# Kernel optimization log

Measured on AMD Instinct MI355X. Metric: run time of the kernel, lower is better.

Reference implementation:

```python
import jax, jax.numpy as jnp
import numpy as np
from jax.scipy.special import logsumexp

B, N, T, D = 32, 400, 315, 512   # batch, fMRI parcels, text/task rows, feature dim
H = 256
EPS = 1e-5                       # InstanceNorm2d default eps
N_ITERS = 100                    # sinkhorn_rpm n_iters


def setup_inputs() -> dict:
    key = jax.random.key(0)
    ks = jax.random.split(key, 6)
    features = jax.random.normal(ks[0], (B, N, D), jnp.float32)
    text = jax.random.normal(ks[1], (T, D), jnp.float32)
    # Affinity bilinear weight, init near identity as in graph-matching Affinity modules
    A = jnp.eye(D, dtype=jnp.float32) + 0.01 * jax.random.normal(ks[2], (D, D), jnp.float32)
    gamma = jnp.ones((), jnp.float32)   # InstanceNorm2d(1, affine=True) weight
    beta = jnp.zeros((), jnp.float32)   # InstanceNorm2d(1, affine=True) bias
    Wh = jax.random.normal(ks[3], (2 * D, H), jnp.float32) / np.float32(np.sqrt(2 * D))
    bh = jnp.zeros((H,), jnp.float32)
    Wo = jax.random.normal(ks[4], (H, 1), jnp.float32) / np.float32(np.sqrt(H))
    bo = jnp.zeros((1,), jnp.float32)
    return {"features": features, "text": text, "A": A, "gamma": gamma,
            "beta": beta, "Wh": Wh, "bh": bh, "Wo": Wo, "bo": bo}


def _forward(features, text, A, gamma, beta, Wh, bh, Wo, bo):
    # Affinity: s[b,n,t] = features[b,n,:] @ A @ text[t,:]   -> [B, N, T]
    s = jnp.einsum('bnd,de,te->bnt', features, A, text)
    # InstanceNorm2d(1, affine): normalize each [N,T] map per batch element (single channel)
    m = jnp.mean(s, axis=(1, 2), keepdims=True)
    v = jnp.var(s, axis=(1, 2), keepdims=True)
    s = gamma * (s - m) * jax.lax.rsqrt(v + EPS) + beta
    # sinkhorn_rpm: log-domain alternating row/col normalization, no slack
    def body(log_a, _):
        log_a = log_a - logsumexp(log_a, axis=2, keepdims=True)  # row normalization
        log_a = log_a - logsumexp(log_a, axis=1, keepdims=True)  # col normalization
        return log_a, None
    log_s, _ = jax.lax.scan(body, s, None, length=N_ITERS)
    s1 = jnp.exp(log_s)                                   # [B, N, T]
    # features_t @ s1, then transpose -> [B, T, D]
    features1 = jnp.einsum('bnd,bnt->btd', features, s1)
    text1 = jnp.broadcast_to(text[None], (features.shape[0], T, D))
    combine = jnp.concatenate([features1, text1], axis=2)  # [B, T, 2D]
    h = jax.nn.relu(combine @ Wh + bh)                     # [B, T, H]
    pred = (h @ Wo + bo)[..., 0]                           # [B, T] == [B, num_tasks]
    return pred


def reference(features, text, A, gamma, beta, Wh, bh, Wo, bo):
    return _forward(features, text, A, gamma, beta, Wh, bh, Wo, bo)
```

## Files before the change

kernel.cpp:

```cpp
#include <hip/hip_runtime.h>
#include <hip/hip_fp16.h>

#define BDIM 32
#define NDIM 400
#define TDIM 315
#define TPAD 320
#define DDIM 512
#define HDIM 256
#define NITER 100

#define OFS_TAB   0u
#define OFS_TB    327680u
#define OFS_WHB   655616u
#define OFS_S1B   9240576u
#define OFS_F1    17432576u
#define OFS_FB    27754496u
#define OFS_QPART (OFS_F1 + 4096u)
#define QSTATS    163840u

typedef __attribute__((ext_vector_type(8))) short bf16x8;
typedef __attribute__((ext_vector_type(4))) float f32x4;
typedef unsigned long long ull;

__device__ __forceinline__ unsigned rne_hi(float x) {
  unsigned u = __float_as_uint(x);
  u += 0x7fffu + ((u >> 16) & 1u);
  return u & 0xffff0000u;
}
__device__ __forceinline__ unsigned pack2(float lo, float hi) {
  return (rne_hi(lo) >> 16) | rne_hi(hi);
}
__device__ __forceinline__ unsigned short bf1(float x) { return (unsigned short)(rne_hi(x) >> 16); }
__device__ __forceinline__ float bfres(float x) {
  return x - __uint_as_float(rne_hi(x));
}

template <int CTRL, int RMASK>
__device__ __forceinline__ float dppadd(float x) {
  int y = __builtin_amdgcn_update_dpp(0, __float_as_int(x), CTRL, RMASK, 0xf, true);
  return x + __int_as_float(y);
}
template <int CTRL, int RMASK>
__device__ __forceinline__ float dppmax(float x) {
  int y = __builtin_amdgcn_update_dpp(0, __float_as_int(x), CTRL, RMASK, 0xf, true);
  return fmaxf(x, __int_as_float(y));
}

#define LDH 40

__global__ __launch_bounds__(256) void k_prep(const float* __restrict__ F,
                                              const float* __restrict__ Wh,
                                              const float* __restrict__ text,
                                              const float* __restrict__ A,
                                              const float* __restrict__ bh,
                                              unsigned short* __restrict__ Fb,
                                              unsigned short* __restrict__ Whb,
                                              unsigned short* __restrict__ tAb,
                                              float* __restrict__ TB,
                                              uint4* __restrict__ qzero) {
  __shared__ unsigned short Ahs[64 * LDH], Als[64 * LDH];
  __shared__ unsigned short Bhs[64 * LDH], Bls[64 * LDH];
  const int bid = blockIdx.x, tid = threadIdx.x;
  if (bid >= 60) {
    const int NF4 = (BDIM * NDIM * DDIM) / 4;
    const int NW4 = (DDIM * HDIM) / 4;
    const int NQ4 = (2 * BDIM * 8 * 320 * 2 + BDIM * 8 * 2 * 2) / 4;
    const int gid = (bid - 60) * 256 + tid;
    const int stride = 452 * 256;
    for (int i = gid; i < NF4; i += stride) {
      float4 v = ((const float4*)F)[i];
      ((uint2*)Fb)[i] = make_uint2(pack2(v.x, v.y), pack2(v.z, v.w));
    }
    for (int i = gid; i < NW4; i += stride) {
      float4 v = ((const float4*)Wh)[i];
      ((uint2*)Whb)[i] = make_uint2(pack2(v.x, v.y), pack2(v.z, v.w));
    }
    for (int i = gid; i < NQ4; i += stride) qzero[i] = make_uint4(0u, 0u, 0u, 0u);
    return;
  }
  const int l = tid & 63, wv = tid >> 6;
  const int m = tid >> 2, kq = (tid & 3) * 8;
  f32x4 acc[4] = {};
  if (bid < 40) {
    const int d0 = (bid & 7) * 64, t0 = (bid >> 3) * 64;
    for (int k0 = 0; k0 < 512; k0 += 32) {
      {
        int t = t0 + m;
        float4 v0 = make_float4(0.f, 0.f, 0.f, 0.f), v1 = v0;
        if (t < TDIM) {
          v0 = *(const float4*)(text + (size_t)t * DDIM + k0 + kq);
          v1 = *(const float4*)(text + (size_t)t * DDIM + k0 + kq + 4);
        }
        *(uint4*)(&Ahs[m * LDH + kq]) =
            make_uint4(pack2(v0.x, v0.y), pack2(v0.z, v0.w), pack2(v1.x, v1.y), pack2(v1.z, v1.w));
        *(uint4*)(&Als[m * LDH + kq]) =
            make_uint4(pack2(bfres(v0.x), bfres(v0.y)), pack2(bfres(v0.z), bfres(v0.w)),
                       pack2(bfres(v1.x), bfres(v1.y)), pack2(bfres(v1.z), bfres(v1.w)));
        float4 w0 = *(const float4*)(A + (size_t)(d0 + m) * DDIM + k0 + kq);
        float4 w1 = *(const float4*)(A + (size_t)(d0 + m) * DDIM + k0 + kq + 4);
        *(uint4*)(&Bhs[m * LDH + kq]) =
            make_uint4(pack2(w0.x, w0.y), pack2(w0.z, w0.w), pack2(w1.x, w1.y), pack2(w1.z, w1.w));
        *(uint4*)(&Bls[m * LDH + kq]) =
            make_uint4(pack2(bfres(w0.x), bfres(w0.y)), pack2(bfres(w0.z), bfres(w0.w)),
                       pack2(bfres(w1.x), bfres(w1.y)), pack2(bfres(w1.z), bfres(w1.w)));
      }
      __syncthreads();
      bf16x8 ah = *(const bf16x8*)(&Ahs[(wv * 16 + (l & 15)) * LDH + (l >> 4) * 8]);
      bf16x8 al = *(const bf16x8*)(&Als[(wv * 16 + (l & 15)) * LDH + (l >> 4) * 8]);
#pragma unroll
      for (int c = 0; c < 4; ++c) {
        bf16x8 bh_ = *(const bf16x8*)(&Bhs[(c * 16 + (l & 15)) * LDH + (l >> 4) * 8]);
        bf16x8 bl_ = *(const bf16x8*)(&Bls[(c * 16 + (l & 15)) * LDH + (l >> 4) * 8]);
        acc[c] = __builtin_amdgcn_mfma_f32_16x16x32_bf16(ah, bh_, acc[c], 0, 0, 0);
        acc[c] = __builtin_amdgcn_mfma_f32_16x16x32_bf16(ah, bl_, acc[c], 0, 0, 0);
        acc[c] = __builtin_amdgcn_mfma_f32_16x16x32_bf16(al, bh_, acc[c], 0, 0, 0);
      }
      __syncthreads();
    }
#pragma unroll
    for (int c = 0; c < 4; ++c)
#pragma unroll
      for (int r = 0; r < 4; ++r) {
        int t = t0 + wv * 16 + ((l >> 4) << 2) + r;
        int d = d0 + c * 16 + (l & 15);
        tAb[(size_t)t * DDIM + d] = bf1(acc[c][r]);
      }
  } else {
    const int idx = bid - 40;
    const int h0 = (idx & 3) * 64, t0 = (idx >> 2) * 64;
    const float* Wb = Wh + DDIM * HDIM;
    const int col = tid & 31, g = tid >> 5;
    for (int k0 = 0; k0 < 512; k0 += 32) {
      {
        int t = t0 + m;
        float4 v0 = make_float4(0.f, 0.f, 0.f, 0.f), v1 = v0;
        if (t < TDIM) {
          v0 = *(const float4*)(text + (size_t)t * DDIM + k0 + kq);
          v1 = *(const float4*)(text + (size_t)t * DDIM + k0 + kq + 4);
        }
        *(uint4*)(&Ahs[m * LDH + kq]) =
            make_uint4(pack2(v0.x, v0.y), pack2(v0.z, v0.w), pack2(v1.x, v1.y), pack2(v1.z, v1.w));
        *(uint4*)(&Als[m * LDH + kq]) =
            make_uint4(pack2(bfres(v0.x), bfres(v0.y)), pack2(bfres(v0.z), bfres(v0.w)),
                       pack2(bfres(v1.x), bfres(v1.y)), pack2(bfres(v1.z), bfres(v1.w)));
        float4 w0 = *(const float4*)(Wb + (size_t)(k0 + col) * HDIM + h0 + g * 8);
        float4 w1 = *(const float4*)(Wb + (size_t)(k0 + col) * HDIM + h0 + g * 8 + 4);
        float wr[8] = {w0.x, w0.y, w0.z, w0.w, w1.x, w1.y, w1.z, w1.w};
#pragma unroll
        for (int i = 0; i < 8; ++i) {
          Bhs[(g * 8 + i) * LDH + col] = bf1(wr[i]);
          Bls[(g * 8 + i) * LDH + col] = bf1(bfres(wr[i]));
        }
      }
      __syncthreads();
      bf16x8 ah = *(const bf16x8*)(&Ahs[(wv * 16 + (l & 15)) * LDH + (l >> 4) * 8]);
      bf16x8 al = *(const bf16x8*)(&Als[(wv * 16 + (l & 15)) * LDH + (l >> 4) * 8]);
#pragma unroll
      for (int c = 0; c < 4; ++c) {
        bf16x8 bh_ = *(const bf16x8*)(&Bhs[(c * 16 + (l & 15)) * LDH + (l >> 4) * 8]);
        bf16x8 bl_ = *(const bf16x8*)(&Bls[(c * 16 + (l & 15)) * LDH + (l >> 4) * 8]);
        acc[c] = __builtin_amdgcn_mfma_f32_16x16x32_bf16(ah, bh_, acc[c], 0, 0, 0);
        acc[c] = __builtin_amdgcn_mfma_f32_16x16x32_bf16(ah, bl_, acc[c], 0, 0, 0);
        acc[c] = __builtin_amdgcn_mfma_f32_16x16x32_bf16(al, bh_, acc[c], 0, 0, 0);
      }
      __syncthreads();
    }
#pragma unroll
    for (int c = 0; c < 4; ++c)
#pragma unroll
      for (int r = 0; r < 4; ++r) {
        int t = t0 + wv * 16 + ((l >> 4) << 2) + r;
        int h = h0 + c * 16 + (l & 15);
        TB[(size_t)t * HDIM + h] = acc[c][r] + bh[h];
      }
  }
}

#define SBLK 8
#define SROWS 50
#define SRPW 10

__global__ __launch_bounds__(320, 1) void k_sinkhorn(const unsigned short* __restrict__ Fb,
                                                     const unsigned short* __restrict__ tAb,
                                                     const float* __restrict__ gptr,
                                                     const float* __restrict__ bptr,
                                                     unsigned short* __restrict__ s1b,
                                                     ull* __restrict__ qpart) {
  __shared__ unsigned short Fch[64 * LDH];
  __shared__ unsigned short tACh[320 * LDH];
  __shared__ float Sls[SROWS * 320];
  __shared__ float qpl[5][320];
  __shared__ float qg[5][320];
  __shared__ float sred[16];
  const int b = blockIdx.x, c = blockIdx.y;
  const int tid = threadIdx.x, wv = tid >> 6, l = tid & 63;
  unsigned short* S1 = s1b + (size_t)b * NDIM * TPAD;
  const unsigned short* Fbb = Fb + (size_t)b * NDIM * DDIM + (size_t)c * SROWS * DDIM;
  const float TOL = 1e-3f;
  const float TN_RATIO = 315.0f / 400.0f;

  f32x4 acc[16] = {};
  {
    const int m = tid >> 2, kq = (tid & 3) * 8;
    for (int k0 = 0; k0 < 512; k0 += 32) {
      if (m < 64) {
        uint4 fv = make_uint4(0, 0, 0, 0);
        if (m < SROWS) fv = *(const uint4*)(Fbb + (size_t)m * DDIM + k0 + kq);
        *(uint4*)(&Fch[m * LDH + kq]) = fv;
      }
#pragma unroll
      for (int p = 0; p < 4; ++p) {
        int row = p * 80 + m;
        *(uint4*)(&tACh[row * LDH + kq]) = *(const uint4*)(tAb + (size_t)row * DDIM + k0 + kq);
      }
      __syncthreads();
      bf16x8 af[4];
#pragma unroll
      for (int nt = 0; nt < 4; ++nt)
        af[nt] = *(const bf16x8*)(&Fch[(nt * 16 + (l & 15)) * LDH + (l >> 4) * 8]);
#pragma unroll
      for (int tt = 0; tt < 4; ++tt) {
        bf16x8 bf_ = *(const bf16x8*)(&tACh[((wv * 4 + tt) * 16 + (l & 15)) * LDH + (l >> 4) * 8]);
#pragma unroll
        for (int nt = 0; nt < 4; ++nt)
          acc[tt * 4 + nt] = __builtin_amdgcn_mfma_f32_16x16x32_bf16(af[nt], bf_, acc[tt * 4 + nt], 0, 0, 0);
      }
      __syncthreads();
    }
  }
  float ls = 0.f, lq = 0.f;
#pragma unroll
  for (int tt = 0; tt < 4; ++tt) {
    int t = (wv * 4 + tt) * 16 + (l & 15);
    bool tv = (t < TDIM);
#pragma unroll
    for (int nt = 0; nt < 4; ++nt)
#pragma unroll
      for (int r = 0; r < 4; ++r) {
        int n = nt * 16 + ((l >> 4) << 2) + r;
        if (n < SROWS && tv) {
          float v = acc[tt * 4 + nt][r];
          Sls[n * 320 + t] = v;
          ls += v;
          lq = fmaf(v, v, lq);
        }
      }
  }
#pragma unroll
  for (int mm = 1; mm <= 32; mm <<= 1) {
    ls += __shfl_xor(ls, mm, 64);
    lq += __shfl_xor(lq, mm, 64);
  }
  if (l == 0) { sred[wv] = ls; sred[8 + wv] = lq; }
  __syncthreads();
  {
    ull* satoms = qpart + QSTATS;
    if (tid == 0) {
      float Ssum = sred[0] + sred[1] + sred[2] + sred[3] + sred[4];
      float Sq = sred[8] + sred[9] + sred[10] + sred[11] + sred[12];
      ull* mine = satoms + ((size_t)b * SBLK + c) * 2;
      __hip_atomic_store(&mine[0], (1ull << 32) | (ull)__float_as_uint(Ssum),
                         __ATOMIC_RELAXED, __HIP_MEMORY_SCOPE_AGENT);
      __hip_atomic_store(&mine[1], (1ull << 32) | (ull)__float_as_uint(Sq),
                         __ATOMIC_RELAXED, __HIP_MEMORY_SCOPE_AGENT);
    }
    if (wv == 0) {
      ull g = (1ull << 32);
      const ull* base = satoms + (size_t)b * SBLK * 2;
      if (l < 16) g = __hip_atomic_load(&base[l], __ATOMIC_RELAXED, __HIP_MEMORY_SCOPE_AGENT);
      int guard = 0;
      while (!((unsigned)(g >> 32) >= 1u)) {
        if (++guard > (1 << 20)) break;
        if (l < 16) g = __hip_atomic_load(&base[l], __ATOMIC_RELAXED, __HIP_MEMORY_SCOPE_AGENT);
      }
      for (;;) {
        if (__ballot((unsigned)(g >> 32) >= 1u) == ~0ull) break;
        if (l < 16 && (unsigned)(g >> 32) < 1u)
          g = __hip_atomic_load(&base[l], __ATOMIC_RELAXED, __HIP_MEMORY_SCOPE_AGENT);
      }
      if (l < 16) sred[l] = __uint_as_float((unsigned)g);
    }
  }
  __syncthreads();
  const float NT = 400.0f * 315.0f;
  const float Ssum_all = ((sred[0] + sred[2]) + (sred[4] + sred[6])) +
                         ((sred[8] + sred[10]) + (sred[12] + sred[14]));
  const float Sq_all = ((sred[1] + sred[3]) + (sred[5] + sred[7])) +
                       ((sred[9] + sred[11]) + (sred[13] + sred[15]));
  const float mean = Ssum_all / NT;
  const float var = Sq_all / NT - mean * mean;
  const float inv = rsqrtf(var + 1e-5f);
  const float alpha = gptr[0] * inv;
  const float L2E = 1.4426950408889634f;
  const float a2 = alpha * L2E;
  const float d2 = (bptr[0] - mean * alpha) * L2E;
  const int r0 = c * SROWS + wv * SRPW;

  float E0[SRPW], E1[SRPW], E2[SRPW], E3[SRPW], E4[SRPW];
#pragma unroll
  for (int j = 0; j < SRPW; ++j) {
    const float* row = Sls + (wv * SRPW + j) * 320;
    E0[j] = __builtin_amdgcn_exp2f(fmaf(row[l], a2, d2));
    E1[j] = __builtin_amdgcn_exp2f(fmaf(row[64 + l], a2, d2));
    E2[j] = __builtin_amdgcn_exp2f(fmaf(row[128 + l], a2, d2));
    E3[j] = __builtin_amdgcn_exp2f(fmaf(row[192 + l], a2, d2));
    E4[j] = (l < 59) ? __builtin_amdgcn_exp2f(fmaf(row[256 + l], a2, d2)) : 0.0f;
  }
  float w0 = 1.0f, w1 = 1.0f, w2 = 1.0f, w3 = 1.0f, w4 = (l < 59) ? 1.0f : 0.0f;
  float aj[SRPW];
#pragma unroll
  for (int j = 0; j < SRPW; ++j) aj[j] = 0.0f;

  bool fin = false;
  for (int it = 0; it < NITER; ++it) {
    float p[SRPW];
#pragma unroll
    for (int j = 0; j < SRPW; ++j) {
      float t = E4[j] * w4;
      t = fmaf(E3[j], w3, t);
      t = fmaf(E2[j], w2, t);
      t = fmaf(E1[j], w1, t);
      p[j] = fmaf(E0[j], w0, t);
    }
#pragma unroll
    for (int j = 0; j < SRPW; ++j) p[j] = dppadd<0x111, 0xf>(p[j]);
#pragma unroll
    for (int j = 0; j < SRPW; ++j) p[j] = dppadd<0x112, 0xf>(p[j]);
#pragma unroll
    for (int j = 0; j < SRPW; ++j) p[j] = dppadd<0x114, 0xf>(p[j]);
#pragma unroll
    for (int j = 0; j < SRPW; ++j) p[j] = dppadd<0x118, 0xf>(p[j]);
#pragma unroll
    for (int j = 0; j < SRPW; ++j) p[j] = dppadd<0x142, 0xa>(p[j]);
#pragma unroll
    for (int j = 0; j < SRPW; ++j) p[j] = dppadd<0x143, 0xc>(p[j]);
#pragma unroll
    for (int j = 0; j < SRPW; ++j) {
      float r = __builtin_amdgcn_rcpf(p[j]);
      aj[j] = __int_as_float(__builtin_amdgcn_readlane(__float_as_int(r), 63));
    }
    float q0 = 0.f, q1 = 0.f, q2 = 0.f, q3 = 0.f, q4 = 0.f;
#pragma unroll
    for (int j = 0; j < SRPW; ++j) {
      q0 = fmaf(E0[j], aj[j], q0);
      q1 = fmaf(E1[j], aj[j], q1);
      q2 = fmaf(E2[j], aj[j], q2);
      q3 = fmaf(E3[j], aj[j], q3);
      q4 = fmaf(E4[j], aj[j], q4);
    }
    qpl[wv][l] = q0;
    qpl[wv][64 + l] = q1;
    qpl[wv][128 + l] = q2;
    qpl[wv][192 + l] = q3;
    qpl[wv][256 + l] = q4;
    __syncthreads();
    const int par = it & 1;
    const unsigned tgt = (unsigned)(it + 1);
    ull* bufpar = qpart + ((size_t)par * BDIM + b) * (SBLK * 320);
    if (wv == 0) {
      ull* myp = bufpar + c * 320;
#pragma unroll
      for (int k = 0; k < 5; ++k) {
        int t = k * 64 + l;
        float sm = qpl[0][t] + qpl[1][t] + qpl[2][t] + qpl[3][t] + qpl[4][t];
        __hip_atomic_store(&myp[t], ((ull)tgt << 32) | (ull)__float_as_uint(sm),
                           __ATOMIC_RELAXED, __HIP_MEMORY_SCOPE_AGENT);
      }
    }
    {
      const int ncc = (wv < 3) ? 2 : 1;
      ull got[2][5];
      const int ccs[2] = {wv, wv + 5};
#pragma unroll
      for (int e = 0; e < 2; ++e)
        if (e < ncc && ccs[e] != c) {
#pragma unroll
          for (int k = 0; k < 5; ++k)
            got[e][k] = __hip_atomic_load(&bufpar[ccs[e] * 320 + k * 64 + l],
                                          __ATOMIC_RELAXED, __HIP_MEMORY_SCOPE_AGENT);
        }
      int guard = 0;
      for (;;) {
        bool ok = true;
#pragma unroll
        for (int e = 0; e < 2; ++e)
          if (e < ncc && ccs[e] != c) {
#pragma unroll
            for (int k = 0; k < 5; ++k)
              if ((unsigned)(got[e][k] >> 32) != tgt) {
                got[e][k] = __hip_atomic_load(&bufpar[ccs[e] * 320 + k * 64 + l],
                                              __ATOMIC_RELAXED, __HIP_MEMORY_SCOPE_AGENT);
                ok = false;
              }
          }
        if (ok) break;
        if (++guard > (1 << 20)) break;
      }
      float part[5] = {0.f, 0.f, 0.f, 0.f, 0.f};
#pragma unroll
      for (int e = 0; e < 2; ++e)
        if (e < ncc) {
#pragma unroll
          for (int k = 0; k < 5; ++k) {
            int t = k * 64 + l;
            float v = (ccs[e] == c)
                          ? (qpl[0][t] + qpl[1][t] + qpl[2][t] + qpl[3][t] + qpl[4][t])
                          : __uint_as_float((unsigned)got[e][k]);
            part[k] += v;
          }
        }
#pragma unroll
      for (int k = 0; k < 5; ++k) qg[wv][k * 64 + l] = part[k];
    }
    __syncthreads();
    const float Q0 = qg[0][l] + qg[1][l] + qg[2][l] + qg[3][l] + qg[4][l];
    const float Q1 = qg[0][64 + l] + qg[1][64 + l] + qg[2][64 + l] + qg[3][64 + l] + qg[4][64 + l];
    const float Q2 =
        qg[0][128 + l] + qg[1][128 + l] + qg[2][128 + l] + qg[3][128 + l] + qg[4][128 + l];
    const float Q3 =
        qg[0][192 + l] + qg[1][192 + l] + qg[2][192 + l] + qg[3][192 + l] + qg[4][192 + l];
    const float Q4 =
        qg[0][256 + l] + qg[1][256 + l] + qg[2][256 + l] + qg[3][256 + l] + qg[4][256 + l];
    float r = fabsf(fmaf(Q0 * w0, TN_RATIO, -1.0f));
    r = fmaxf(r, fabsf(fmaf(Q1 * w1, TN_RATIO, -1.0f)));
    r = fmaxf(r, fabsf(fmaf(Q2 * w2, TN_RATIO, -1.0f)));
    r = fmaxf(r, fabsf(fmaf(Q3 * w3, TN_RATIO, -1.0f)));
    if (l < 59) r = fmaxf(r, fabsf(fmaf(Q4 * w4, TN_RATIO, -1.0f)));
    w0 = __builtin_amdgcn_rcpf(Q0);
    w1 = __builtin_amdgcn_rcpf(Q1);
    w2 = __builtin_amdgcn_rcpf(Q2);
    w3 = __builtin_amdgcn_rcpf(Q3);
    if (l < 59) w4 = __builtin_amdgcn_rcpf(Q4);
    if (fin) break;
    r = dppmax<0x111, 0xf>(r);
    r = dppmax<0x112, 0xf>(r);
    r = dppmax<0x114, 0xf>(r);
    r = dppmax<0x118, 0xf>(r);
    r = dppmax<0x142, 0xa>(r);
    r = dppmax<0x143, 0xc>(r);
    const float resid = __int_as_float(__builtin_amdgcn_readlane(__float_as_int(r), 63));
    fin = (resid < TOL) || (it == NITER - 2);
  }

#pragma unroll
  for (int j = 0; j < SRPW; ++j) {
    unsigned short* row = S1 + (size_t)(r0 + j) * TPAD;
    const float a = aj[j];
    row[l] = bf1(a * E0[j] * w0);
    row[64 + l] = bf1(a * E1[j] * w1);
    row[128 + l] = bf1(a * E2[j] * w2);
    row[192 + l] = bf1(a * E3[j] * w3);
    row[256 + l] = (l < 59) ? bf1(a * E4[j] * w4) : (unsigned short)0;
  }
}

__global__ __launch_bounds__(256) void k_f1(const unsigned short* __restrict__ s1b,
                                            const unsigned short* __restrict__ Fb,
                                            unsigned short* __restrict__ f1b) {
  __shared__ unsigned short Abf[64 * LDH];
  __shared__ unsigned short Bbf[64 * LDH];
  const int tid = threadIdx.x, l = tid & 63, wv = tid >> 6;
  const int bz = blockIdx.x, d0 = blockIdx.y * 64, t0 = blockIdx.z * 64;
  const unsigned short* sb = s1b + (size_t)bz * NDIM * TPAD;
  const unsigned short* Fbb = Fb + (size_t)bz * NDIM * DDIM;
  unsigned short* out = f1b + (size_t)bz * TDIM * DDIM;
  f32x4 acc[4] = {};
  const int col = tid & 31, g = tid >> 5;
  for (int k0 = 0; k0 < 416; k0 += 32) {
    int n = k0 + col;
    uint4 av = make_uint4(0, 0, 0, 0), bv = av;
    if (n < NDIM) {
      av = *(const uint4*)(sb + (size_t)n * TPAD + t0 + g * 8);
      bv = *(const uint4*)(Fbb + (size_t)n * DDIM + d0 + g * 8);
    }
    unsigned short ah[8], bh8[8];
    *(uint4*)ah = av;
    *(uint4*)bh8 = bv;
#pragma unroll
    for (int i = 0; i < 8; ++i) {
      Abf[(g * 8 + i) * LDH + col] = ah[i];
      Bbf[(g * 8 + i) * LDH + col] = bh8[i];
    }
    __syncthreads();
    bf16x8 af = *(const bf16x8*)(&Abf[(wv * 16 + (l & 15)) * LDH + (l >> 4) * 8]);
#pragma unroll
    for (int c = 0; c < 4; ++c) {
      bf16x8 bf_ = *(const bf16x8*)(&Bbf[(c * 16 + (l & 15)) * LDH + (l >> 4) * 8]);
      acc[c] = __builtin_amdgcn_mfma_f32_16x16x32_bf16(af, bf_, acc[c], 0, 0, 0);
    }
    __syncthreads();
  }
#pragma unroll
  for (int c = 0; c < 4; ++c)
#pragma unroll
    for (int r = 0; r < 4; ++r) {
      int t = t0 + wv * 16 + ((l >> 4) << 2) + r;
      int d = d0 + c * 16 + (l & 15);
      if (t < TDIM) out[(size_t)t * DDIM + d] = bf1(acc[c][r]);
    }
}

__global__ __launch_bounds__(256) void k_hp(const unsigned short* __restrict__ f1b,
                                            const unsigned short* __restrict__ Whb,
                                            const float* __restrict__ TB,
                                            const float* __restrict__ Wo,
                                            const float* __restrict__ bo,
                                            float* __restrict__ out) {
  __shared__ unsigned short Abf[64 * LDH];
  __shared__ unsigned short Bbf[256 * LDH];
  __shared__ float Wos[256];
  const int tid = threadIdx.x, l = tid & 63, wv = tid >> 6;
  const int r0 = blockIdx.x * 64;
  const int RTOT = BDIM * TDIM;
  Wos[tid] = Wo[tid];
  f32x4 acc[16] = {};
  const int m = tid >> 2, kq = (tid & 3) * 8;
  const int col = tid & 31, g = tid >> 5;
  for (int k0 = 0; k0 < 512; k0 += 32) {
    uint4 av = make_uint4(0, 0, 0, 0);
    int r = r0 + m;
    if (r < RTOT) av = *(const uint4*)(f1b + (size_t)r * DDIM + k0 + kq);
    *(uint4*)(&Abf[m * LDH + kq]) = av;
#pragma unroll
    for (int p = 0; p < 4; ++p) {
      uint4 bv = *(const uint4*)(Whb + (size_t)(k0 + col) * HDIM + p * 64 + g * 8);
      unsigned short bh8[8];
      *(uint4*)bh8 = bv;
#pragma unroll
      for (int i = 0; i < 8; ++i) Bbf[(p * 64 + g * 8 + i) * LDH + col] = bh8[i];
    }
    __syncthreads();
    bf16x8 af = *(const bf16x8*)(&Abf[(wv * 16 + (l & 15)) * LDH + (l >> 4) * 8]);
#pragma unroll
    for (int c = 0; c < 16; ++c) {
      bf16x8 bf_ = *(const bf16x8*)(&Bbf[(c * 16 + (l & 15)) * LDH + (l >> 4) * 8]);
      acc[c] = __builtin_amdgcn_mfma_f32_16x16x32_bf16(af, bf_, acc[c], 0, 0, 0);
    }
    __syncthreads();
  }
  int tmod[4];
#pragma unroll
  for (int r = 0; r < 4; ++r) {
    int rr = r0 + wv * 16 + ((l >> 4) << 2) + r;
    tmod[r] = rr % TDIM;
  }
  float part[4] = {0.f, 0.f, 0.f, 0.f};
#pragma unroll
  for (int c = 0; c < 16; ++c) {
    int jl = c * 16 + (l & 15);
    float woc = Wos[jl];
#pragma unroll
    for (int r = 0; r < 4; ++r) {
      float v = acc[c][r] + TB[(size_t)tmod[r] * HDIM + jl];
      part[r] = fmaf(fmaxf(v, 0.f), woc, part[r]);
    }
  }
#pragma unroll
  for (int r = 0; r < 4; ++r) part[r] = dppadd<0x111, 0xf>(part[r]);
#pragma unroll
  for (int r = 0; r < 4; ++r) part[r] = dppadd<0x112, 0xf>(part[r]);
#pragma unroll
  for (int r = 0; r < 4; ++r) part[r] = dppadd<0x114, 0xf>(part[r]);
#pragma unroll
  for (int r = 0; r < 4; ++r) part[r] = dppadd<0x118, 0xf>(part[r]);
  if ((l & 15) == 15) {
    const float base = bo[0];
#pragma unroll
    for (int r = 0; r < 4; ++r) {
      int rr = r0 + wv * 16 + ((l >> 4) << 2) + r;
      if (rr < RTOT) out[rr] = part[r] + base;
    }
  }
}

extern "C" void kernel_launch(void* const* d_in, const int* in_sizes, int n_in,
                              void* d_out, int out_size, void* d_ws, size_t ws_size,
                              hipStream_t stream) {
  const float* F     = (const float*)d_in[0];
  const float* text  = (const float*)d_in[1];
  const float* A     = (const float*)d_in[2];
  const float* gamma = (const float*)d_in[3];
  const float* beta  = (const float*)d_in[4];
  const float* Wh    = (const float*)d_in[5];
  const float* bh    = (const float*)d_in[6];
  const float* Wo    = (const float*)d_in[7];
  const float* bo    = (const float*)d_in[8];
  float* out = (float*)d_out;
  char* ws = (char*)d_ws;
  unsigned short* tAb = (unsigned short*)(ws + OFS_TAB);
  float* TB    = (float*)(ws + OFS_TB);
  unsigned short* Whb = (unsigned short*)(ws + OFS_WHB);
  unsigned short* s1b = (unsigned short*)(ws + OFS_S1B);
  unsigned short* f1b = (unsigned short*)(ws + OFS_F1);
  unsigned short* Fb  = (unsigned short*)(ws + OFS_FB);
  ull* qpart = (ull*)(ws + OFS_QPART);

  k_prep<<<512, 256, 0, stream>>>(F, Wh, text, A, bh, Fb, Whb, tAb, TB, (uint4*)qpart);
  k_sinkhorn<<<dim3(BDIM, SBLK), 320, 0, stream>>>(Fb, tAb, gamma, beta, s1b, qpart);
  k_f1<<<dim3(32, 8, 5), 256, 0, stream>>>(s1b, Fb, f1b);
  k_hp<<<dim3(158), 256, 0, stream>>>(f1b, Whb, TB, Wo, bo, out);
}
```

Measured before the change: 185.8 us.

## Fuse features1 GEMM with regression head and pre-transpose operands for MFMA

Merges the features^T·s1 GEMM and the MLP head into one kernel, so the features1 tile stays in LDS and never makes a global round trip. The prep kernel now writes features and Wh as bf16 in transposed, chunked layouts. This lets the fused kernel load its MFMA operands with vector copies instead of scalar LDS transposes. Sinkhorn reads fp32 features directly and converts them itself, and it writes s1 transposed per 50-row chunk through LDS. The risks are that the fused kernel's large LDS and register footprint lowers occupancy and runs only 160 blocks, and that the spin-wait loop was restructured.

```diff
diff --git a/kernel.cpp b/kernel.cpp
--- a/kernel.cpp
+++ b/kernel.cpp
@@ -11,12 +11,11 @@
 
 #define OFS_TAB   0u
 #define OFS_TB    327680u
-#define OFS_WHB   655616u
-#define OFS_S1B   9240576u
-#define OFS_F1    17432576u
-#define OFS_FB    27754496u
-#define OFS_QPART (OFS_F1 + 4096u)
+#define OFS_WHT   655360u
+#define OFS_QPART 917504u
 #define QSTATS    163840u
+#define OFS_S1T   2232320u
+#define OFS_FBT   12718080u
 
 typedef __attribute__((ext_vector_type(8))) short bf16x8;
 typedef __attribute__((ext_vector_type(4))) float f32x4;
@@ -47,35 +46,82 @@
 }
 
 #define LDH 40
+#define SBLK 8
+#define SROWS 50
+#define SRPW 10
 
 __global__ __launch_bounds__(256) void k_prep(const float* __restrict__ F,
                                               const float* __restrict__ Wh,
                                               const float* __restrict__ text,
                                               const float* __restrict__ A,
                                               const float* __restrict__ bh,
-                                              unsigned short* __restrict__ Fb,
-                                              unsigned short* __restrict__ Whb,
                                               unsigned short* __restrict__ tAb,
                                               float* __restrict__ TB,
+                                              unsigned short* __restrict__ WhbT,
+                                              unsigned short* __restrict__ FbT,
                                               uint4* __restrict__ qzero) {
   __shared__ unsigned short Ahs[64 * LDH], Als[64 * LDH];
   __shared__ unsigned short Bhs[64 * LDH], Bls[64 * LDH];
+  __shared__ float Tls[64 * 69];
   const int bid = blockIdx.x, tid = threadIdx.x;
   if (bid >= 60) {
-    const int NF4 = (BDIM * NDIM * DDIM) / 4;
-    const int NW4 = (DDIM * HDIM) / 4;
-    const int NQ4 = (2 * BDIM * 8 * 320 * 2 + BDIM * 8 * 2 * 2) / 4;
-    const int gid = (bid - 60) * 256 + tid;
-    const int stride = 452 * 256;
-    for (int i = gid; i < NF4; i += stride) {
-      float4 v = ((const float4*)F)[i];
-      ((uint2*)Fb)[i] = make_uint2(pack2(v.x, v.y), pack2(v.z, v.w));
-    }
-    for (int i = gid; i < NW4; i += stride) {
-      float4 v = ((const float4*)Wh)[i];
-      ((uint2*)Whb)[i] = make_uint2(pack2(v.x, v.y), pack2(v.z, v.w));
-    }
-    for (int i = gid; i < NQ4; i += stride) qzero[i] = make_uint4(0u, 0u, 0u, 0u);
+    if (bid < 316) {
+      const int bb = (bid - 60) >> 3, cc = (bid - 60) & 7;
+      const float* Fs = F + ((size_t)bb * NDIM + cc * SROWS) * DDIM;
+      unsigned short* Ft = FbT + (size_t)(bb * SBLK + cc) * DDIM * 64;
+      for (int d0 = 0; d0 < DDIM; d0 += 64) {
+        for (int idx = tid; idx < 800; idx += 256) {
+          int nr = idx >> 4, q = idx & 15;
+          float4 v = *(const float4*)(Fs + (size_t)nr * DDIM + d0 + q * 4);
+          Tls[nr * 69 + q * 4 + 0] = v.x;
+          Tls[nr * 69 + q * 4 + 1] = v.y;
+          Tls[nr * 69 + q * 4 + 2] = v.z;
+          Tls[nr * 69 + q * 4 + 3] = v.w;
+        }
+        __syncthreads();
+#pragma unroll
+        for (int p = 0; p < 2; ++p) {
+          int idx = p * 256 + tid;
+          int dr = idx >> 3, oct = idx & 7;
+          unsigned short us[8];
+#pragma unroll
+          for (int i = 0; i < 8; ++i) {
+            int n = oct * 8 + i;
+            us[i] = (n < SROWS) ? bf1(Tls[n * 69 + dr]) : (unsigned short)0;
+          }
+          *(uint4*)(Ft + (size_t)(d0 + dr) * 64 + oct * 8) = *(uint4*)us;
+        }
+        __syncthreads();
+      }
+      return;
+    }
+    if (bid < 348) {
+      const int ti = bid - 316;
+      const int k0 = (ti & 7) * 64, j0 = (ti >> 3) * 64;
+      for (int idx = tid; idx < 1024; idx += 256) {
+        int kr = idx >> 4, q = idx & 15;
+        float4 v = *(const float4*)(Wh + (size_t)(k0 + kr) * HDIM + j0 + q * 4);
+        Tls[kr * 69 + q * 4 + 0] = v.x;
+        Tls[kr * 69 + q * 4 + 1] = v.y;
+        Tls[kr * 69 + q * 4 + 2] = v.z;
+        Tls[kr * 69 + q * 4 + 3] = v.w;
+      }
+      __syncthreads();
+#pragma unroll
+      for (int p = 0; p < 2; ++p) {
+        int idx = p * 256 + tid;
+        int jr = idx >> 3, oct = idx & 7;
+        unsigned short us[8];
+#pragma unroll
+        for (int i = 0; i < 8; ++i) us[i] = bf1(Tls[(oct * 8 + i) * 69 + jr]);
+        *(uint4*)(WhbT + (size_t)(j0 + jr) * DDIM + k0 + oct * 8) = *(uint4*)us;
+      }
+      return;
+    }
+    const int NQ16 = 82176;
+    const int gid = (bid - 348) * 256 + tid;
+    const int stride = 164 * 256;
+    for (int i = gid; i < NQ16; i += stride) qzero[i] = make_uint4(0u, 0u, 0u, 0u);
     return;
   }
   const int l = tid & 63, wv = tid >> 6;
@@ -176,15 +222,11 @@
   }
 }
 
-#define SBLK 8
-#define SROWS 50
-#define SRPW 10
-
-__global__ __launch_bounds__(320, 1) void k_sinkhorn(const unsigned short* __restrict__ Fb,
+__global__ __launch_bounds__(320, 1) void k_sinkhorn(const float* __restrict__ F,
                                                      const unsigned short* __restrict__ tAb,
                                                      const float* __restrict__ gptr,
                                                      const float* __restrict__ bptr,
-                                                     unsigned short* __restrict__ s1b,
+                                                     unsigned short* __restrict__ s1T,
                                                      ull* __restrict__ qpart) {
   __shared__ unsigned short Fch[64 * LDH];
   __shared__ unsigned short tACh[320 * LDH];
@@ -194,8 +236,7 @@
   __shared__ float sred[16];
   const int b = blockIdx.x, c = blockIdx.y;
   const int tid = threadIdx.x, wv = tid >> 6, l = tid & 63;
-  unsigned short* S1 = s1b + (size_t)b * NDIM * TPAD;
-  const unsigned short* Fbb = Fb + (size_t)b * NDIM * DDIM + (size_t)c * SROWS * DDIM;
+  const float* Fs = F + ((size_t)b * NDIM + (size_t)c * SROWS) * DDIM;
   const float TOL = 1e-3f;
   const float TN_RATIO = 315.0f / 400.0f;
 
@@ -205,7 +246,12 @@
     for (int k0 = 0; k0 < 512; k0 += 32) {
       if (m < 64) {
         uint4 fv = make_uint4(0, 0, 0, 0);
-        if (m < SROWS) fv = *(const uint4*)(Fbb + (size_t)m * DDIM + k0 + kq);
+        if (m < SROWS) {
+          float4 v0 = *(const float4*)(Fs + (size_t)m * DDIM + k0 + kq);
+          float4 v1 = *(const float4*)(Fs + (size_t)m * DDIM + k0 + kq + 4);
+          fv = make_uint4(pack2(v0.x, v0.y), pack2(v0.z, v0.w),
+                          pack2(v1.x, v1.y), pack2(v1.z, v1.w));
+        }
         *(uint4*)(&Fch[m * LDH + kq]) = fv;
       }
 #pragma unroll
@@ -269,12 +315,9 @@
       const ull* base = satoms + (size_t)b * SBLK * 2;
       if (l < 16) g = __hip_atomic_load(&base[l], __ATOMIC_RELAXED, __HIP_MEMORY_SCOPE_AGENT);
       int guard = 0;
-      while (!((unsigned)(g >> 32) >= 1u)) {
-        if (++guard > (1 << 20)) break;
-        if (l < 16) g = __hip_atomic_load(&base[l], __ATOMIC_RELAXED, __HIP_MEMORY_SCOPE_AGENT);
-      }
       for (;;) {
         if (__ballot((unsigned)(g >> 32) >= 1u) == ~0ull) break;
+        if (++guard > (1 << 20)) break;
         if (l < 16 && (unsigned)(g >> 32) < 1u)
           g = __hip_atomic_load(&base[l], __ATOMIC_RELAXED, __HIP_MEMORY_SCOPE_AGENT);
       }
@@ -294,7 +337,6 @@
   const float L2E = 1.4426950408889634f;
   const float a2 = alpha * L2E;
   const float d2 = (bptr[0] - mean * alpha) * L2E;
-  const int r0 = c * SROWS + wv * SRPW;
 
   float E0[SRPW], E1[SRPW], E2[SRPW], E3[SRPW], E4[SRPW];
 #pragma unroll
@@ -442,134 +484,148 @@
     fin = (resid < TOL) || (it == NITER - 2);
   }
 
-#pragma unroll
-  for (int j = 0; j < SRPW; ++j) {
-    unsigned short* row = S1 + (size_t)(r0 + j) * TPAD;
-    const float a = aj[j];
-    row[l] = bf1(a * E0[j] * w0);
-    row[64 + l] = bf1(a * E1[j] * w1);
-    row[128 + l] = bf1(a * E2[j] * w2);
-    row[192 + l] = bf1(a * E3[j] * w3);
-    row[256 + l] = (l < 59) ? bf1(a * E4[j] * w4) : (unsigned short)0;
-  }
-}
-
-__global__ __launch_bounds__(256) void k_f1(const unsigned short* __restrict__ s1b,
-                                            const unsigned short* __restrict__ Fb,
-                                            unsigned short* __restrict__ f1b) {
+  {
+    unsigned short* SlsT = (unsigned short*)Sls;
+#pragma unroll
+    for (int j = 0; j < SRPW; ++j) {
+      const int n = wv * SRPW + j;
+      const float a = aj[j];
+      SlsT[(size_t)l * 72 + n] = bf1(a * E0[j] * w0);
+      SlsT[(size_t)(64 + l) * 72 + n] = bf1(a * E1[j] * w1);
+      SlsT[(size_t)(128 + l) * 72 + n] = bf1(a * E2[j] * w2);
+      SlsT[(size_t)(192 + l) * 72 + n] = bf1(a * E3[j] * w3);
+      SlsT[(size_t)(256 + l) * 72 + n] = (l < 59) ? bf1(a * E4[j] * w4) : (unsigned short)0;
+    }
+    for (int i = tid; i < 320 * 14; i += 320) {
+      int t = i / 14, n = 50 + (i % 14);
+      SlsT[(size_t)t * 72 + n] = 0;
+    }
+    __syncthreads();
+    unsigned short* S1c = s1T + (size_t)(b * SBLK + c) * 320 * 64;
+    for (int i = tid; i < 320 * 8; i += 320) {
+      int row = i >> 3, oct = i & 7;
+      *(uint4*)(S1c + (size_t)row * 64 + oct * 8) =
+          *(const uint4*)(SlsT + (size_t)row * 72 + oct * 8);
+    }
+  }
+}
+
+__global__ __launch_bounds__(256) void k_out(const unsigned short* __restrict__ s1T,
+                                             const unsigned short* __restrict__ FbT,
+                                             const unsigned short* __restrict__ WhbT,
+                                             const float* __restrict__ TB,
+                                             const float* __restrict__ Wo,
+                                             const float* __restrict__ bo,
+                                             float* __restrict__ out) {
   __shared__ unsigned short Abf[64 * LDH];
-  __shared__ unsigned short Bbf[64 * LDH];
+  __shared__ unsigned short Bbf[512 * LDH];
+  __shared__ unsigned short f1L[64 * 520];
+  __shared__ float Wos[256];
+  __shared__ float predp[4][64];
+  const int b = blockIdx.x, t0 = blockIdx.y * 64;
   const int tid = threadIdx.x, l = tid & 63, wv = tid >> 6;
-  const int bz = blockIdx.x, d0 = blockIdx.y * 64, t0 = blockIdx.z * 64;
-  const unsigned short* sb = s1b + (size_t)bz * NDIM * TPAD;
-  const unsigned short* Fbb = Fb + (size_t)bz * NDIM * DDIM;
-  unsigned short* out = f1b + (size_t)bz * TDIM * DDIM;
-  f32x4 acc[4] = {};
-  const int col = tid & 31, g = tid >> 5;
-  for (int k0 = 0; k0 < 416; k0 += 32) {
-    int n = k0 + col;
-    uint4 av = make_uint4(0, 0, 0, 0), bv = av;
-    if (n < NDIM) {
-      av = *(const uint4*)(sb + (size_t)n * TPAD + t0 + g * 8);
-      bv = *(const uint4*)(Fbb + (size_t)n * DDIM + d0 + g * 8);
-    }
-    unsigned short ah[8], bh8[8];
-    *(uint4*)ah = av;
-    *(uint4*)bh8 = bv;
-#pragma unroll
-    for (int i = 0; i < 8; ++i) {
-      Abf[(g * 8 + i) * LDH + col] = ah[i];
-      Bbf[(g * 8 + i) * LDH + col] = bh8[i];
+  Wos[tid] = Wo[tid];
+  const unsigned short* S1b = s1T + (size_t)b * SBLK * 320 * 64;
+  const unsigned short* Fbt = FbT + (size_t)b * SBLK * DDIM * 64;
+  const int m = tid >> 2, kq = (tid & 3) * 8;
+  f32x4 acc[32] = {};
+  for (int ch = 0; ch < 16; ++ch) {
+    const int c = ch >> 1, h = ch & 1;
+    *(uint4*)(&Abf[m * LDH + kq]) =
+        *(const uint4*)(S1b + ((size_t)c * 320 + t0 + m) * 64 + h * 32 + kq);
+#pragma unroll
+    for (int p = 0; p < 8; ++p) {
+      int idx = p * 256 + tid;
+      int d = idx >> 2, q = idx & 3;
+      *(uint4*)(&Bbf[d * LDH + q * 8]) =
+          *(const uint4*)(Fbt + ((size_t)c * DDIM + d) * 64 + h * 32 + q * 8);
     }
     __syncthreads();
-    bf16x8 af = *(const bf16x8*)(&Abf[(wv * 16 + (l & 15)) * LDH + (l >> 4) * 8]);
-#pragma unroll
-    for (int c = 0; c < 4; ++c) {
-      bf16x8 bf_ = *(const bf16x8*)(&Bbf[(c * 16 + (l & 15)) * LDH + (l >> 4) * 8]);
-      acc[c] = __builtin_amdgcn_mfma_f32_16x16x32_bf16(af, bf_, acc[c], 0, 0, 0);
+    bf16x8 af[4];
+#pragma unroll
+    for (int tt = 0; tt < 4; ++tt)
+      af[tt] = *(const bf16x8*)(&Abf[(tt * 16 + (l & 15)) * LDH + (l >> 4) * 8]);
+#pragma unroll
+    for (int dt = 0; dt < 8; ++dt) {
+      bf16x8 bf_ = *(const bf16x8*)(&Bbf[(wv * 128 + dt * 16 + (l & 15)) * LDH + (l >> 4) * 8]);
+#pragma unroll
+      for (int tt = 0; tt < 4; ++tt)
+        acc[tt * 8 + dt] =
+            __builtin_amdgcn_mfma_f32_16x16x32_bf16(af[tt], bf_, acc[tt * 8 + dt], 0, 0, 0);
     }
     __syncthreads();
   }
 #pragma unroll
-  for (int c = 0; c < 4; ++c)
-#pragma unroll
-    for (int r = 0; r < 4; ++r) {
-      int t = t0 + wv * 16 + ((l >> 4) << 2) + r;
-      int d = d0 + c * 16 + (l & 15);
-      if (t < TDIM) out[(size_t)t * DDIM + d] = bf1(acc[c][r]);
-    }
-}
-
-__global__ __launch_bounds__(256) void k_hp(const unsigned short* __restrict__ f1b,
-                                            const unsigned short* __restrict__ Whb,
-                                            const float* __restrict__ TB,
-                                            const float* __restrict__ Wo,
-                                            const float* __restrict__ bo,
-                                            float* __restrict__ out) {
-  __shared__ unsigned short Abf[64 * LDH];
-  __shared__ unsigned short Bbf[256 * LDH];
-  __shared__ float Wos[256];
-  const int tid = threadIdx.x, l = tid & 63, wv = tid >> 6;
-  const int r0 = blockIdx.x * 64;
-  const int RTOT = BDIM * TDIM;
-  Wos[tid] = Wo[tid];
-  f32x4 acc[16] = {};
-  const int m = tid >> 2, kq = (tid & 3) * 8;
-  const int col = tid & 31, g = tid >> 5;
+  for (int tt = 0; tt < 4; ++tt)
+#pragma unroll
+    for (int dt = 0; dt < 8; ++dt)
+#pragma unroll
+      for (int r = 0; r < 4; ++r) {
+        int t_loc = tt * 16 + ((l >> 4) << 2) + r;
+        int d = wv * 128 + dt * 16 + (l & 15);
+        f1L[t_loc * 520 + d] = bf1(acc[tt * 8 + dt][r]);
+      }
+  __syncthreads();
+  f32x4 acc2[16] = {};
   for (int k0 = 0; k0 < 512; k0 += 32) {
-    uint4 av = make_uint4(0, 0, 0, 0);
-    int r = r0 + m;
-    if (r < RTOT) av = *(const uint4*)(f1b + (size_t)r * DDIM + k0 + kq);
-    *(uint4*)(&Abf[m * LDH + kq]) = av;
 #pragma unroll
     for (int p = 0; p < 4; ++p) {
-      uint4 bv = *(const uint4*)(Whb + (size_t)(k0 + col) * HDIM + p * 64 + g * 8);
-      unsigned short bh8[8];
-      *(uint4*)bh8 = bv;
-#pragma unroll
-      for (int i = 0; i < 8; ++i) Bbf[(p * 64 + g * 8 + i) * LDH + col] = bh8[i];
+      int idx = p * 256 + tid;
+      int j = idx >> 2, q = idx & 3;
+      *(uint4*)(&Bbf[j * LDH + q * 8]) = *(const uint4*)(WhbT + (size_t)j * DDIM + k0 + q * 8);
     }
     __syncthreads();
-    bf16x8 af = *(const bf16x8*)(&Abf[(wv * 16 + (l & 15)) * LDH + (l >> 4) * 8]);
-#pragma unroll
-    for (int c = 0; c < 16; ++c) {
-      bf16x8 bf_ = *(const bf16x8*)(&Bbf[(c * 16 + (l & 15)) * LDH + (l >> 4) * 8]);
-      acc[c] = __builtin_amdgcn_mfma_f32_16x16x32_bf16(af, bf_, acc[c], 0, 0, 0);
+    bf16x8 af2[4];
+#pragma unroll
+    for (int rt = 0; rt < 4; ++rt)
+      af2[rt] = *(const bf16x8*)(&f1L[(rt * 16 + (l & 15)) * 520 + (l >> 4) * 8 + k0]);
+#pragma unroll
+    for (int jt = 0; jt < 4; ++jt) {
+      bf16x8 bf_ = *(const bf16x8*)(&Bbf[(wv * 64 + jt * 16 + (l & 15)) * LDH + (l >> 4) * 8]);
+#pragma unroll
+      for (int rt = 0; rt < 4; ++rt)
+        acc2[rt * 4 + jt] =
+            __builtin_amdgcn_mfma_f32_16x16x32_bf16(af2[rt], bf_, acc2[rt * 4 + jt], 0, 0, 0);
     }
     __syncthreads();
   }
-  int tmod[4];
-#pragma unroll
-  for (int r = 0; r < 4; ++r) {
-    int rr = r0 + wv * 16 + ((l >> 4) << 2) + r;
-    tmod[r] = rr % TDIM;
-  }
-  float part[4] = {0.f, 0.f, 0.f, 0.f};
-#pragma unroll
-  for (int c = 0; c < 16; ++c) {
-    int jl = c * 16 + (l & 15);
-    float woc = Wos[jl];
-#pragma unroll
-    for (int r = 0; r < 4; ++r) {
-      float v = acc[c][r] + TB[(size_t)tmod[r] * HDIM + jl];
-      part[r] = fmaf(fmaxf(v, 0.f), woc, part[r]);
-    }
-  }
-#pragma unroll
-  for (int r = 0; r < 4; ++r) part[r] = dppadd<0x111, 0xf>(part[r]);
-#pragma unroll
-  for (int r = 0; r < 4; ++r) part[r] = dppadd<0x112, 0xf>(part[r]);
-#pragma unroll
-  for (int r = 0; r < 4; ++r) part[r] = dppadd<0x114, 0xf>(part[r]);
-#pragma unroll
-  for (int r = 0; r < 4; ++r) part[r] = dppadd<0x118, 0xf>(part[r]);
+  float part[16];
+#pragma unroll
+  for (int i = 0; i < 16; ++i) part[i] = 0.f;
+#pragma unroll
+  for (int jt = 0; jt < 4; ++jt) {
+    int j = wv * 64 + jt * 16 + (l & 15);
+    float woc = Wos[j];
+#pragma unroll
+    for (int rt = 0; rt < 4; ++rt)
+#pragma unroll
+      for (int r = 0; r < 4; ++r) {
+        int t = t0 + rt * 16 + ((l >> 4) << 2) + r;
+        float v = acc2[rt * 4 + jt][r] + TB[(size_t)t * HDIM + j];
+        part[rt * 4 + r] = fmaf(fmaxf(v, 0.f), woc, part[rt * 4 + r]);
+      }
+  }
+#pragma unroll
+  for (int i = 0; i < 16; ++i) part[i] = dppadd<0x111, 0xf>(part[i]);
+#pragma unroll
+  for (int i = 0; i < 16; ++i) part[i] = dppadd<0x112, 0xf>(part[i]);
+#pragma unroll
+  for (int i = 0; i < 16; ++i) part[i] = dppadd<0x114, 0xf>(part[i]);
+#pragma unroll
+  for (int i = 0; i < 16; ++i) part[i] = dppadd<0x118, 0xf>(part[i]);
   if ((l & 15) == 15) {
-    const float base = bo[0];
-#pragma unroll
-    for (int r = 0; r < 4; ++r) {
-      int rr = r0 + wv * 16 + ((l >> 4) << 2) + r;
-      if (rr < RTOT) out[rr] = part[r] + base;
-    }
+#pragma unroll
+    for (int rt = 0; rt < 4; ++rt)
+#pragma unroll
+      for (int r = 0; r < 4; ++r)
+        predp[wv][rt * 16 + ((l >> 4) << 2) + r] = part[rt * 4 + r];
+  }
+  __syncthreads();
+  if (tid < 64) {
+    int t = t0 + tid;
+    if (t < TDIM)
+      out[(size_t)b * TDIM + t] =
+          predp[0][tid] + predp[1][tid] + predp[2][tid] + predp[3][tid] + bo[0];
   }
 }
 
@@ -587,16 +643,14 @@
   const float* bo    = (const float*)d_in[8];
   float* out = (float*)d_out;
   char* ws = (char*)d_ws;
-  unsigned short* tAb = (unsigned short*)(ws + OFS_TAB);
-  float* TB    = (float*)(ws + OFS_TB);
-  unsigned short* Whb = (unsigned short*)(ws + OFS_WHB);
-  unsigned short* s1b = (unsigned short*)(ws + OFS_S1B);
-  unsigned short* f1b = (unsigned short*)(ws + OFS_F1);
-  unsigned short* Fb  = (unsigned short*)(ws + OFS_FB);
-  ull* qpart = (ull*)(ws + OFS_QPART);
-
-  k_prep<<<512, 256, 0, stream>>>(F, Wh, text, A, bh, Fb, Whb, tAb, TB, (uint4*)qpart);
-  k_sinkhorn<<<dim3(BDIM, SBLK), 320, 0, stream>>>(Fb, tAb, gamma, beta, s1b, qpart);
-  k_f1<<<dim3(32, 8, 5), 256, 0, stream>>>(s1b, Fb, f1b);
-  k_hp<<<dim3(158), 256, 0, stream>>>(f1b, Whb, TB, Wo, bo, out);
-}
+  unsigned short* tAb  = (unsigned short*)(ws + OFS_TAB);
+  float* TB     = (float*)(ws + OFS_TB);
+  unsigned short* WhbT = (unsigned short*)(ws + OFS_WHT);
+  ull* qpart    = (ull*)(ws + OFS_QPART);
+  unsigned short* s1T  = (unsigned short*)(ws + OFS_S1T);
+  unsigned short* FbT  = (unsigned short*)(ws + OFS_FBT);
+
+  k_prep<<<512, 256, 0, stream>>>(F, Wh, text, A, bh, tAb, TB, WhbT, FbT, (uint4*)qpart);
+  k_sinkhorn<<<dim3(BDIM, SBLK), 320, 0, stream>>>(F, tAb, gamma, beta, s1T, qpart);
+  k_out<<<dim3(BDIM, 5), 256, 0, stream>>>(s1T, FbT, WhbT, TB, Wo, bo, out);
+}
```

Measured after the change: 178.8 us, median of 2. 1.04x faster.
